# Optimization experiments

Measured on AMD Instinct MI355X. Metric: run time of the kernel, lower is better.

## Reference

```python
import jax, jax.numpy as jnp
import numpy as np

WS = 7       # window_size
NH = 6       # num_heads
DIM = 192
HD = DIM // NH
SCALE = HD ** -0.5


def setup_inputs() -> dict:
    key = jax.random.key(0)
    ks = jax.random.split(key, 9)
    x = jax.random.normal(ks[0], (64, 56, 56, DIM), dtype=jnp.float32)
    s = DIM ** -0.5
    Wq = jax.random.normal(ks[1], (DIM, DIM), dtype=jnp.float32) * s
    bq = jax.random.normal(ks[2], (DIM,), dtype=jnp.float32) * 0.01
    Wk = jax.random.normal(ks[3], (DIM, DIM), dtype=jnp.float32) * s
    bk = jax.random.normal(ks[4], (DIM,), dtype=jnp.float32) * 0.01
    Wv = jax.random.normal(ks[5], (DIM, DIM), dtype=jnp.float32) * s
    bv = jax.random.normal(ks[6], (DIM,), dtype=jnp.float32) * 0.01
    Wo = jax.random.normal(ks[7], (DIM, DIM), dtype=jnp.float32) * s
    bo = jax.random.normal(ks[8], (DIM,), dtype=jnp.float32) * 0.01
    return {"x": x, "Wq": Wq, "bq": bq, "Wk": Wk, "bk": bk,
            "Wv": Wv, "bv": bv, "Wo": Wo, "bo": bo}


def reference(x, Wq, bq, Wk, bk, Wv, bv, Wo, bo):
    B, H, W, C = x.shape
    pad_h = (WS - H % WS) % WS
    pad_w = (WS - W % WS) % WS
    xp = jnp.pad(x, ((0, 0), (0, pad_h), (0, pad_w), (0, 0)))
    Hp, Wp = H + pad_h, W + pad_w
    nH, nW = Hp // WS, Wp // WS
    L = WS * WS  # tokens per window (49)
    # window partition: [B*nH*nW, L, C]
    xw = xp.reshape(B, nH, WS, nW, WS, C).transpose(0, 1, 3, 2, 4, 5).reshape(-1, L, C)
    q = (xw @ Wq + bq).reshape(-1, L, NH, HD)
    k = (xw @ Wk + bk).reshape(-1, L, NH, HD)
    v = (xw @ Wv + bv).reshape(-1, L, NH, HD)
    attn = jnp.einsum('wlhd,wmhd->whlm', q, k) * SCALE  # [nWin, NH, L, L]
    attn = jax.nn.softmax(attn, axis=-1)
    out = jnp.einsum('whlm,wmhd->wlhd', attn, v).reshape(-1, L, C)
    # window reverse
    out = out.reshape(B, nH, nW, WS, WS, C).transpose(0, 1, 3, 2, 4, 5).reshape(B, Hp, Wp, C)
    out = out[:, :H, :W, :]
    return out @ Wo + bo
```

## Files before the change

kernel.cpp:

```cpp
#include <hip/hip_runtime.h>

typedef __bf16 bf16;
typedef __bf16 bf16x8 __attribute__((ext_vector_type(8)));
typedef __bf16 bf16x4 __attribute__((ext_vector_type(4)));
typedef float  f32x4  __attribute__((ext_vector_type(4)));

#define SCALE 0.17677669529663687f

#define PQKV_OFF 0
#define PWO_OFF  221184
#define BQKV_OFF 294912
#define BO_OFF   297216

__global__ __launch_bounds__(256)
void prep_kernel(const float* __restrict__ Wq, const float* __restrict__ bq,
                 const float* __restrict__ Wk, const float* __restrict__ bk,
                 const float* __restrict__ Wv, const float* __restrict__ bv,
                 const float* __restrict__ Wo, const float* __restrict__ bo,
                 bf16* __restrict__ pqkv, bf16* __restrict__ pwo,
                 float* __restrict__ bqkv, float* __restrict__ boc)
{
    int idx = blockIdx.x * 256 + threadIdx.x;
    if (idx < 110592) {
        int j = idx & 7, lane = (idx >> 3) & 63, kb = (idx >> 9) % 6, nt = idx / 3072;
        int n = nt * 16 + (lane & 15);
        int k = kb * 32 + ((lane >> 4) << 3) + j;
        float v;
        if (n < 192)      v = Wq[k * 192 + n];
        else if (n < 384) v = Wk[k * 192 + (n - 192)];
        else              v = Wv[k * 192 + (n - 384)];
        pqkv[idx] = (bf16)v;
    } else if (idx < 110592 + 36864) {
        int p = idx - 110592;
        int j = p & 7, lane = (p >> 3) & 63, kb = (p >> 9) % 6, nt = p / 3072;
        int n = nt * 16 + (lane & 15);
        int k = kb * 32 + ((lane >> 4) << 3) + j;
        pwo[p] = (bf16)Wo[k * 192 + n];
    } else if (idx < 110592 + 36864 + 576) {
        int p = idx - 110592 - 36864;
        float v = (p < 192) ? bq[p] : (p < 384) ? bk[p - 192] : bv[p - 384];
        bqkv[p] = v;
    } else if (idx < 110592 + 36864 + 576 + 192) {
        int p = idx - 110592 - 36864 - 576;
        boc[p] = bo[p];
    }
}


__global__ __launch_bounds__(512, 1)
void winattn_kernel(const float* __restrict__ x,
                    const bf16* __restrict__ pqkv, const bf16* __restrict__ pwo,
                    const float* __restrict__ bqkv, const float* __restrict__ boc,
                    float* __restrict__ out)
{
    extern __shared__ char smem_raw[];
    bf16* xo = (bf16*)smem_raw;
    bf16* q  = xo + 64 * 200;
    bf16* kk = q  + 64 * 200;
    bf16* vT = kk + 64 * 200;
    bf16* pl = vT + 192 * 72;

    const int tid  = threadIdx.x;
    const int w    = tid >> 6;
    const int lane = tid & 63;
    const int quad = lane >> 4;
    const int ln   = lane & 15;

    const int blk = blockIdx.x;
    const int b   = blk >> 6;
    const int rem = blk & 63;
    const int h0  = (rem >> 3) * 7;
    const int w0  = (rem & 7) * 7;
    const float* xbase = x   + ((size_t)(b * 56 + h0) * 56 + w0) * 192;
    float*       obase = out + ((size_t)(b * 56 + h0) * 56 + w0) * 192;

    for (int i = tid; i < 64 * 48; i += 512) {
        int row = i / 48;
        int c4  = (i % 48) * 4;
        f32x4 v = {0.f, 0.f, 0.f, 0.f};
        if (row < 49) {
            const float* p = xbase + ((row / 7) * 56 + (row % 7)) * 192 + c4;
            v = *(const f32x4*)p;
        }
        bf16x4 hv;
        hv[0] = (bf16)v[0]; hv[1] = (bf16)v[1]; hv[2] = (bf16)v[2]; hv[3] = (bf16)v[3];
        *(bf16x4*)&xo[row * 200 + c4] = hv;
    }
    __syncthreads();

    {
        const int mt0 = (w >> 2) * 2;
        const int cw  = w & 3;
        f32x4 acc[2][9];
        #pragma unroll
        for (int mt = 0; mt < 2; mt++)
            #pragma unroll
            for (int i = 0; i < 9; i++) acc[mt][i] = (f32x4){0.f, 0.f, 0.f, 0.f};

        #pragma unroll
        for (int kb = 0; kb < 6; kb++) {
            bf16x8 A[2];
            #pragma unroll
            for (int mt = 0; mt < 2; mt++)
                A[mt] = *(const bf16x8*)&xo[((mt0 + mt) * 16 + ln) * 200 + kb * 32 + quad * 8];
            #pragma unroll
            for (int i = 0; i < 9; i++) {
                int nt = cw + 4 * i;
                bf16x8 B = *(const bf16x8*)&pqkv[((nt * 6 + kb) * 64 + lane) * 8];
                #pragma unroll
                for (int mt = 0; mt < 2; mt++)
                    acc[mt][i] = __builtin_amdgcn_mfma_f32_16x16x32_bf16(A[mt], B, acc[mt][i], 0, 0, 0);
            }
        }
        #pragma unroll
        for (int i = 0; i < 9; i++) {
            int nt = cw + 4 * i;
            int n  = nt * 16 + ln;
            float bias = bqkv[n];
            if (n < 192) {
                #pragma unroll
                for (int mt = 0; mt < 2; mt++)
                    #pragma unroll
                    for (int r = 0; r < 4; r++)
                        q[((mt0 + mt) * 16 + quad * 4 + r) * 200 + n] = (bf16)(acc[mt][i][r] + bias);
            } else if (n < 384) {
                #pragma unroll
                for (int mt = 0; mt < 2; mt++)
                    #pragma unroll
                    for (int r = 0; r < 4; r++)
                        kk[((mt0 + mt) * 16 + quad * 4 + r) * 200 + (n - 192)] = (bf16)(acc[mt][i][r] + bias);
            } else {
                #pragma unroll
                for (int mt = 0; mt < 2; mt++) {
                    bf16x4 hv;
                    #pragma unroll
                    for (int r = 0; r < 4; r++) hv[r] = (bf16)(acc[mt][i][r] + bias);
                    *(bf16x4*)&vT[(n - 384) * 72 + (mt0 + mt) * 16 + quad * 4] = hv;
                }
            }
        }
    }
    __syncthreads();

    {
        const int rt = w >> 1;
        const int hg = w & 1;
        bf16* pw = pl + w * (16 * 72);
        #pragma unroll 1
        for (int h = hg; h < 6; h += 2) {
            bf16x8 aq = *(const bf16x8*)&q[(rt * 16 + ln) * 200 + h * 32 + quad * 8];
            f32x4 s[4];
            #pragma unroll
            for (int nt = 0; nt < 4; nt++) {
                bf16x8 bk8 = *(const bf16x8*)&kk[(nt * 16 + ln) * 200 + h * 32 + quad * 8];
                s[nt] = __builtin_amdgcn_mfma_f32_16x16x32_bf16(aq, bk8, (f32x4){0.f, 0.f, 0.f, 0.f}, 0, 0, 0);
            }
            float rmax[4] = {-1e30f, -1e30f, -1e30f, -1e30f};
            #pragma unroll
            for (int nt = 0; nt < 4; nt++) {
                int col = nt * 16 + ln;
                #pragma unroll
                for (int r = 0; r < 4; r++) {
                    float v = s[nt][r] * SCALE;
                    v = (col < 49) ? v : -1e30f;
                    s[nt][r] = v;
                    rmax[r] = fmaxf(rmax[r], v);
                }
            }
            #pragma unroll
            for (int xm = 1; xm < 16; xm <<= 1)
                #pragma unroll
                for (int r = 0; r < 4; r++)
                    rmax[r] = fmaxf(rmax[r], __shfl_xor(rmax[r], xm, 64));
            float rsum[4] = {0.f, 0.f, 0.f, 0.f};
            #pragma unroll
            for (int nt = 0; nt < 4; nt++)
                #pragma unroll
                for (int r = 0; r < 4; r++) {
                    float p = __expf(s[nt][r] - rmax[r]);
                    s[nt][r] = p;
                    rsum[r] += p;
                }
            #pragma unroll
            for (int xm = 1; xm < 16; xm <<= 1)
                #pragma unroll
                for (int r = 0; r < 4; r++)
                    rsum[r] += __shfl_xor(rsum[r], xm, 64);
            #pragma unroll
            for (int nt = 0; nt < 4; nt++)
                #pragma unroll
                for (int r = 0; r < 4; r++)
                    pw[(quad * 4 + r) * 72 + nt * 16 + ln] = (bf16)s[nt][r];

            float rinv[4];
            #pragma unroll
            for (int r = 0; r < 4; r++) rinv[r] = 1.0f / rsum[r];

            bf16x8 ap0 = *(const bf16x8*)&pw[ln * 72 + quad * 8];
            bf16x8 ap1 = *(const bf16x8*)&pw[ln * 72 + 32 + quad * 8];
            #pragma unroll
            for (int nt2 = 0; nt2 < 2; nt2++) {
                f32x4 o = {0.f, 0.f, 0.f, 0.f};
                bf16x8 bv0 = *(const bf16x8*)&vT[(h * 32 + nt2 * 16 + ln) * 72 + quad * 8];
                bf16x8 bv1 = *(const bf16x8*)&vT[(h * 32 + nt2 * 16 + ln) * 72 + 32 + quad * 8];
                o = __builtin_amdgcn_mfma_f32_16x16x32_bf16(ap0, bv0, o, 0, 0, 0);
                o = __builtin_amdgcn_mfma_f32_16x16x32_bf16(ap1, bv1, o, 0, 0, 0);
                #pragma unroll
                for (int r = 0; r < 4; r++)
                    xo[(rt * 16 + quad * 4 + r) * 200 + h * 32 + nt2 * 16 + ln] = (bf16)(o[r] * rinv[r]);
            }
        }
    }
    __syncthreads();

    {
        const int mt0 = (w >> 2) * 2;
        const int ntb = (w & 3) * 3;
        f32x4 acc[2][3];
        #pragma unroll
        for (int mt = 0; mt < 2; mt++)
            #pragma unroll
            for (int i = 0; i < 3; i++) acc[mt][i] = (f32x4){0.f, 0.f, 0.f, 0.f};

        #pragma unroll
        for (int kb = 0; kb < 6; kb++) {
            bf16x8 A[2];
            #pragma unroll
            for (int mt = 0; mt < 2; mt++)
                A[mt] = *(const bf16x8*)&xo[((mt0 + mt) * 16 + ln) * 200 + kb * 32 + quad * 8];
            #pragma unroll
            for (int i = 0; i < 3; i++) {
                int nt = ntb + i;
                bf16x8 B = *(const bf16x8*)&pwo[((nt * 6 + kb) * 64 + lane) * 8];
                #pragma unroll
                for (int mt = 0; mt < 2; mt++)
                    acc[mt][i] = __builtin_amdgcn_mfma_f32_16x16x32_bf16(A[mt], B, acc[mt][i], 0, 0, 0);
            }
        }
        #pragma unroll
        for (int i = 0; i < 3; i++) {
            int nt = ntb + i;
            int n  = nt * 16 + ln;
            float bias = boc[n];
            #pragma unroll
            for (int mt = 0; mt < 2; mt++)
                #pragma unroll
                for (int r = 0; r < 4; r++) {
                    int l = (mt0 + mt) * 16 + quad * 4 + r;
                    if (l < 49)
                        obase[((l / 7) * 56 + (l % 7)) * 192 + n] = acc[mt][i][r] + bias;
                }
        }
    }
}

extern "C" void kernel_launch(void* const* d_in, const int* in_sizes, int n_in,
                              void* d_out, int out_size, void* d_ws, size_t ws_size,
                              hipStream_t stream)
{
    const float* x  = (const float*)d_in[0];
    const float* Wq = (const float*)d_in[1];
    const float* bq = (const float*)d_in[2];
    const float* Wk = (const float*)d_in[3];
    const float* bk = (const float*)d_in[4];
    const float* Wv = (const float*)d_in[5];
    const float* bv = (const float*)d_in[6];
    const float* Wo = (const float*)d_in[7];
    const float* bo = (const float*)d_in[8];
    float* out = (float*)d_out;

    bf16*  pqkv = (bf16*)((char*)d_ws + PQKV_OFF);
    bf16*  pwo  = (bf16*)((char*)d_ws + PWO_OFF);
    float* bqkv = (float*)((char*)d_ws + BQKV_OFF);
    float* boc  = (float*)((char*)d_ws + BO_OFF);

    prep_kernel<<<579, 256, 0, stream>>>(Wq, bq, Wk, bk, Wv, bv, Wo, bo,
                                         pqkv, pwo, bqkv, boc);

    const size_t smem = (size_t)(64 * 200 * 3 + 192 * 72 + 8 * 16 * 72) * sizeof(bf16);
    winattn_kernel<<<4096, 512, smem, stream>>>(x, pqkv, pwo, bqkv, boc, out);
}
```

Baseline: 520.2 us.

## Load x straight into MFMA fragments, drop P staging, raise occupancy

The x tile is now read from global memory directly into bf16 MFMA A-fragments held in registers, so the shared-memory staging buffer and one barrier go away. The QKV projection is split into three chunks to keep accumulator register pressure down. Attention computes S^T (K as the A operand), so the softmax reduction needs only two cross-lane shuffles, and P is rearranged with ds_bpermute instead of a round trip through LDS. The attention output reuses the q buffer, which shrinks LDS use enough for launch bounds to request 4 blocks per CU. The costs are more global load instructions per lane, permute overhead, and possible spilling under the tighter register budget.

```diff
diff --git a/kernel.cpp b/kernel.cpp
--- a/kernel.cpp
+++ b/kernel.cpp
@@ -46,19 +46,24 @@
     }
 }
 
-
-__global__ __launch_bounds__(512, 1)
+__device__ inline unsigned pack2(float a, float b)
+{
+    union { bf16 h[2]; unsigned u; } t;
+    t.h[0] = (bf16)a; t.h[1] = (bf16)b;
+    return t.u;
+}
+
+
+__global__ __launch_bounds__(512, 4)
 void winattn_kernel(const float* __restrict__ x,
                     const bf16* __restrict__ pqkv, const bf16* __restrict__ pwo,
                     const float* __restrict__ bqkv, const float* __restrict__ boc,
                     float* __restrict__ out)
 {
     extern __shared__ char smem_raw[];
-    bf16* xo = (bf16*)smem_raw;
-    bf16* q  = xo + 64 * 200;
+    bf16* q  = (bf16*)smem_raw;
     bf16* kk = q  + 64 * 200;
     bf16* vT = kk + 64 * 200;
-    bf16* pl = vT + 192 * 72;
 
     const int tid  = threadIdx.x;
     const int w    = tid >> 6;
@@ -74,68 +79,72 @@
     const float* xbase = x   + ((size_t)(b * 56 + h0) * 56 + w0) * 192;
     float*       obase = out + ((size_t)(b * 56 + h0) * 56 + w0) * 192;
 
-    for (int i = tid; i < 64 * 48; i += 512) {
-        int row = i / 48;
-        int c4  = (i % 48) * 4;
-        f32x4 v = {0.f, 0.f, 0.f, 0.f};
-        if (row < 49) {
-            const float* p = xbase + ((row / 7) * 56 + (row % 7)) * 192 + c4;
-            v = *(const f32x4*)p;
-        }
-        bf16x4 hv;
-        hv[0] = (bf16)v[0]; hv[1] = (bf16)v[1]; hv[2] = (bf16)v[2]; hv[3] = (bf16)v[3];
-        *(bf16x4*)&xo[row * 200 + c4] = hv;
-    }
-    __syncthreads();
-
     {
         const int mt0 = (w >> 2) * 2;
         const int cw  = w & 3;
-        f32x4 acc[2][9];
-        #pragma unroll
-        for (int mt = 0; mt < 2; mt++)
-            #pragma unroll
-            for (int i = 0; i < 9; i++) acc[mt][i] = (f32x4){0.f, 0.f, 0.f, 0.f};
-
-        #pragma unroll
-        for (int kb = 0; kb < 6; kb++) {
-            bf16x8 A[2];
+
+        bf16x8 Afr[2][6];
+        #pragma unroll
+        for (int mt = 0; mt < 2; mt++) {
+            int wr = (mt0 + mt) * 16 + ln;
+            bool valid = wr < 49;
+            int wrc = valid ? wr : 0;
+            const float* rp_ = xbase + ((wrc / 7) * 56 + (wrc % 7)) * 192;
+            #pragma unroll
+            for (int kb = 0; kb < 6; kb++) {
+                f32x4 a0 = *(const f32x4*)(rp_ + kb * 32 + quad * 8);
+                f32x4 a1 = *(const f32x4*)(rp_ + kb * 32 + quad * 8 + 4);
+                if (!valid) { a0 = (f32x4){0.f,0.f,0.f,0.f}; a1 = (f32x4){0.f,0.f,0.f,0.f}; }
+                bf16x8 fr;
+                #pragma unroll
+                for (int j = 0; j < 4; j++) { fr[j] = (bf16)a0[j]; fr[4 + j] = (bf16)a1[j]; }
+                Afr[mt][kb] = fr;
+            }
+        }
+
+        #pragma unroll 1
+        for (int c = 0; c < 3; c++) {
+            f32x4 acc[2][3];
             #pragma unroll
             for (int mt = 0; mt < 2; mt++)
-                A[mt] = *(const bf16x8*)&xo[((mt0 + mt) * 16 + ln) * 200 + kb * 32 + quad * 8];
-            #pragma unroll
-            for (int i = 0; i < 9; i++) {
-                int nt = cw + 4 * i;
-                bf16x8 B = *(const bf16x8*)&pqkv[((nt * 6 + kb) * 64 + lane) * 8];
-                #pragma unroll
-                for (int mt = 0; mt < 2; mt++)
-                    acc[mt][i] = __builtin_amdgcn_mfma_f32_16x16x32_bf16(A[mt], B, acc[mt][i], 0, 0, 0);
-            }
-        }
-        #pragma unroll
-        for (int i = 0; i < 9; i++) {
-            int nt = cw + 4 * i;
-            int n  = nt * 16 + ln;
-            float bias = bqkv[n];
-            if (n < 192) {
-                #pragma unroll
-                for (int mt = 0; mt < 2; mt++)
+                #pragma unroll
+                for (int i = 0; i < 3; i++) acc[mt][i] = (f32x4){0.f,0.f,0.f,0.f};
+
+            #pragma unroll
+            for (int i = 0; i < 3; i++) {
+                int nt = cw + 4 * (c * 3 + i);
+                #pragma unroll
+                for (int kb = 0; kb < 6; kb++) {
+                    bf16x8 B = *(const bf16x8*)&pqkv[((nt * 6 + kb) * 64 + lane) * 8];
+                    acc[0][i] = __builtin_amdgcn_mfma_f32_16x16x32_bf16(Afr[0][kb], B, acc[0][i], 0, 0, 0);
+                    acc[1][i] = __builtin_amdgcn_mfma_f32_16x16x32_bf16(Afr[1][kb], B, acc[1][i], 0, 0, 0);
+                }
+            }
+            #pragma unroll
+            for (int i = 0; i < 3; i++) {
+                int nt = cw + 4 * (c * 3 + i);
+                int n  = nt * 16 + ln;
+                float bias = bqkv[n];
+                if (n < 192) {
                     #pragma unroll
-                    for (int r = 0; r < 4; r++)
-                        q[((mt0 + mt) * 16 + quad * 4 + r) * 200 + n] = (bf16)(acc[mt][i][r] + bias);
-            } else if (n < 384) {
-                #pragma unroll
-                for (int mt = 0; mt < 2; mt++)
+                    for (int mt = 0; mt < 2; mt++)
+                        #pragma unroll
+                        for (int r = 0; r < 4; r++)
+                            q[((mt0 + mt) * 16 + quad * 4 + r) * 200 + n] = (bf16)(acc[mt][i][r] + bias);
+                } else if (n < 384) {
                     #pragma unroll
-                    for (int r = 0; r < 4; r++)
-                        kk[((mt0 + mt) * 16 + quad * 4 + r) * 200 + (n - 192)] = (bf16)(acc[mt][i][r] + bias);
-            } else {
-                #pragma unroll
-                for (int mt = 0; mt < 2; mt++) {
-                    bf16x4 hv;
+                    for (int mt = 0; mt < 2; mt++)
+                        #pragma unroll
+                        for (int r = 0; r < 4; r++)
+                            kk[((mt0 + mt) * 16 + quad * 4 + r) * 200 + (n - 192)] = (bf16)(acc[mt][i][r] + bias);
+                } else {
                     #pragma unroll
-                    for (int r = 0; r < 4; r++) hv[r] = (bf16)(acc[mt][i][r] + bias);
-                    *(bf16x4*)&vT[(n - 384) * 72 + (mt0 + mt) * 16 + quad * 4] = hv;
+                    for (int mt = 0; mt < 2; mt++) {
+                        bf16x4 hv;
+                        #pragma unroll
+                        for (int r = 0; r < 4; r++) hv[r] = (bf16)(acc[mt][i][r] + bias);
+                        *(bf16x4*)&vT[(n - 384) * 72 + (mt0 + mt) * 16 + quad * 4] = hv;
+                    }
                 }
             }
         }
@@ -145,92 +154,97 @@
     {
         const int rt = w >> 1;
         const int hg = w & 1;
-        bf16* pw = pl + w * (16 * 72);
+        const int idxA = (((lane & 16) >> 4) * 32 + ln) * 4;
+        const int idxB = idxA + 64;
+
         #pragma unroll 1
         for (int h = hg; h < 6; h += 2) {
-            bf16x8 aq = *(const bf16x8*)&q[(rt * 16 + ln) * 200 + h * 32 + quad * 8];
+            bf16x8 bq8 = *(const bf16x8*)&q[(rt * 16 + ln) * 200 + h * 32 + quad * 8];
             f32x4 s[4];
             #pragma unroll
             for (int nt = 0; nt < 4; nt++) {
-                bf16x8 bk8 = *(const bf16x8*)&kk[(nt * 16 + ln) * 200 + h * 32 + quad * 8];
-                s[nt] = __builtin_amdgcn_mfma_f32_16x16x32_bf16(aq, bk8, (f32x4){0.f, 0.f, 0.f, 0.f}, 0, 0, 0);
-            }
-            float rmax[4] = {-1e30f, -1e30f, -1e30f, -1e30f};
-            #pragma unroll
-            for (int nt = 0; nt < 4; nt++) {
-                int col = nt * 16 + ln;
+                bf16x8 ak = *(const bf16x8*)&kk[(nt * 16 + ln) * 200 + h * 32 + quad * 8];
+                s[nt] = __builtin_amdgcn_mfma_f32_16x16x32_bf16(ak, bq8, (f32x4){0.f,0.f,0.f,0.f}, 0, 0, 0);
+            }
+            float m = -1e30f;
+            #pragma unroll
+            for (int nt = 0; nt < 4; nt++)
                 #pragma unroll
                 for (int r = 0; r < 4; r++) {
                     float v = s[nt][r] * SCALE;
-                    v = (col < 49) ? v : -1e30f;
+                    v = (nt * 16 + quad * 4 + r < 49) ? v : -1e30f;
                     s[nt][r] = v;
-                    rmax[r] = fmaxf(rmax[r], v);
-                }
-            }
-            #pragma unroll
-            for (int xm = 1; xm < 16; xm <<= 1)
-                #pragma unroll
-                for (int r = 0; r < 4; r++)
-                    rmax[r] = fmaxf(rmax[r], __shfl_xor(rmax[r], xm, 64));
-            float rsum[4] = {0.f, 0.f, 0.f, 0.f};
+                    m = fmaxf(m, v);
+                }
+            m = fmaxf(m, __shfl_xor(m, 16, 64));
+            m = fmaxf(m, __shfl_xor(m, 32, 64));
+            float sum = 0.f;
             #pragma unroll
             for (int nt = 0; nt < 4; nt++)
                 #pragma unroll
                 for (int r = 0; r < 4; r++) {
-                    float p = __expf(s[nt][r] - rmax[r]);
+                    float p = __expf(s[nt][r] - m);
                     s[nt][r] = p;
-                    rsum[r] += p;
-                }
-            #pragma unroll
-            for (int xm = 1; xm < 16; xm <<= 1)
-                #pragma unroll
-                for (int r = 0; r < 4; r++)
-                    rsum[r] += __shfl_xor(rsum[r], xm, 64);
+                    sum += p;
+                }
+            sum += __shfl_xor(sum, 16, 64);
+            sum += __shfl_xor(sum, 32, 64);
+            float rinv = 1.0f / sum;
             #pragma unroll
             for (int nt = 0; nt < 4; nt++)
                 #pragma unroll
-                for (int r = 0; r < 4; r++)
-                    pw[(quad * 4 + r) * 72 + nt * 16 + ln] = (bf16)s[nt][r];
-
-            float rinv[4];
-            #pragma unroll
-            for (int r = 0; r < 4; r++) rinv[r] = 1.0f / rsum[r];
-
-            bf16x8 ap0 = *(const bf16x8*)&pw[ln * 72 + quad * 8];
-            bf16x8 ap1 = *(const bf16x8*)&pw[ln * 72 + 32 + quad * 8];
+                for (int r = 0; r < 4; r++) s[nt][r] *= rinv;
+
+            unsigned pk[4][2];
+            #pragma unroll
+            for (int nt = 0; nt < 4; nt++) {
+                pk[nt][0] = pack2(s[nt][0], s[nt][1]);
+                pk[nt][1] = pack2(s[nt][2], s[nt][3]);
+            }
+            union { unsigned u[4]; bf16x8 v; } ap[2];
+            #pragma unroll
+            for (int ntA = 0; ntA < 2; ntA++)
+                #pragma unroll
+                for (int w2 = 0; w2 < 4; w2++) {
+                    int idx = (w2 < 2) ? idxA : idxB;
+                    unsigned lo = __builtin_amdgcn_ds_bpermute(idx, (int)pk[2 * ntA][w2 & 1]);
+                    unsigned hi = __builtin_amdgcn_ds_bpermute(idx, (int)pk[2 * ntA + 1][w2 & 1]);
+                    ap[ntA].u[w2] = (quad & 2) ? hi : lo;
+                }
+
             #pragma unroll
             for (int nt2 = 0; nt2 < 2; nt2++) {
                 f32x4 o = {0.f, 0.f, 0.f, 0.f};
                 bf16x8 bv0 = *(const bf16x8*)&vT[(h * 32 + nt2 * 16 + ln) * 72 + quad * 8];
                 bf16x8 bv1 = *(const bf16x8*)&vT[(h * 32 + nt2 * 16 + ln) * 72 + 32 + quad * 8];
-                o = __builtin_amdgcn_mfma_f32_16x16x32_bf16(ap0, bv0, o, 0, 0, 0);
-                o = __builtin_amdgcn_mfma_f32_16x16x32_bf16(ap1, bv1, o, 0, 0, 0);
+                o = __builtin_amdgcn_mfma_f32_16x16x32_bf16(ap[0].v, bv0, o, 0, 0, 0);
+                o = __builtin_amdgcn_mfma_f32_16x16x32_bf16(ap[1].v, bv1, o, 0, 0, 0);
                 #pragma unroll
                 for (int r = 0; r < 4; r++)
-                    xo[(rt * 16 + quad * 4 + r) * 200 + h * 32 + nt2 * 16 + ln] = (bf16)(o[r] * rinv[r]);
+                    q[(rt * 16 + quad * 4 + r) * 200 + h * 32 + nt2 * 16 + ln] = (bf16)o[r];
             }
         }
     }
     __syncthreads();
 
     {
-        const int mt0 = (w >> 2) * 2;
-        const int ntb = (w & 3) * 3;
+        const int mt0  = (w >> 2) * 2;
+        const int ntb4 = (w & 3) * 3;
         f32x4 acc[2][3];
         #pragma unroll
         for (int mt = 0; mt < 2; mt++)
             #pragma unroll
-            for (int i = 0; i < 3; i++) acc[mt][i] = (f32x4){0.f, 0.f, 0.f, 0.f};
+            for (int i = 0; i < 3; i++) acc[mt][i] = (f32x4){0.f,0.f,0.f,0.f};
 
         #pragma unroll
         for (int kb = 0; kb < 6; kb++) {
             bf16x8 A[2];
             #pragma unroll
             for (int mt = 0; mt < 2; mt++)
-                A[mt] = *(const bf16x8*)&xo[((mt0 + mt) * 16 + ln) * 200 + kb * 32 + quad * 8];
+                A[mt] = *(const bf16x8*)&q[((mt0 + mt) * 16 + ln) * 200 + kb * 32 + quad * 8];
             #pragma unroll
             for (int i = 0; i < 3; i++) {
-                int nt = ntb + i;
+                int nt = ntb4 + i;
                 bf16x8 B = *(const bf16x8*)&pwo[((nt * 6 + kb) * 64 + lane) * 8];
                 #pragma unroll
                 for (int mt = 0; mt < 2; mt++)
@@ -239,7 +253,7 @@
         }
         #pragma unroll
         for (int i = 0; i < 3; i++) {
-            int nt = ntb + i;
+            int nt = ntb4 + i;
             int n  = nt * 16 + ln;
             float bias = boc[n];
             #pragma unroll
@@ -277,6 +291,6 @@
     prep_kernel<<<579, 256, 0, stream>>>(Wq, bq, Wk, bk, Wv, bv, Wo, bo,
                                          pqkv, pwo, bqkv, boc);
 
-    const size_t smem = (size_t)(64 * 200 * 3 + 192 * 72 + 8 * 16 * 72) * sizeof(bf16);
+    const size_t smem = (size_t)(64 * 200 * 2 + 192 * 72) * sizeof(bf16);
     winattn_kernel<<<4096, 512, smem, stream>>>(x, pqkv, pwo, bqkv, boc, out);
 }
```

Measured after the change: 456.3 us. -12.3%, faster.
